# Performance work log

Hardware: AMD Instinct MI355X
Metric: run time of the kernel (lower is better)

## Reference

```python
import jax, jax.numpy as jnp
import numpy as np

LN_EPS = 1e-5


def setup_inputs() -> dict:
    key = jax.random.key(0)
    k1, k2, k3, k4, k5, k6 = jax.random.split(key, 6)
    B, S, P = 4, 4096, 16          # batch, seq_len, max_n_bytes
    LR, D = 256, 1024              # lowrank_dim, embedding_dim
    # byte ids in [-1, 255]; -1 marks missing bytes
    bytes_ids = jax.random.randint(k1, (B, S, P), -1, 256)
    byte_table = jax.random.normal(k2, (256, LR), dtype=jnp.float32) * 0.02
    pos_emb = jax.random.normal(k3, (P, LR, LR), dtype=jnp.float32)
    W_up = jax.random.normal(k4, (D, LR), dtype=jnp.float32) * 0.02
    b_up = jnp.zeros((D,), dtype=jnp.float32)
    ln_gamma = jnp.ones((D,), dtype=jnp.float32)
    ln_beta = jnp.zeros((D,), dtype=jnp.float32)
    return {
        "bytes_ids": bytes_ids,
        "byte_table": byte_table,
        "pos_emb": pos_emb,
        "W_up": W_up,
        "b_up": b_up,
        "ln_gamma": ln_gamma,
        "ln_beta": ln_beta,
    }


def reference(bytes_ids, byte_table, pos_emb, W_up, b_up, ln_gamma, ln_beta):
    # bytes_ids: [B, S, P] int, -1 => missing byte
    missing = bytes_ids == -1                             # [B,S,P]
    ids = jnp.where(missing, 0, bytes_ids)
    be = byte_table[ids]                                  # [B,S,P,LR] gather
    # per-position small matmul: pos_emb[p] applied to each byte embedding
    emb = jnp.einsum('pij,bspi->bspj', pos_emb, be)       # [B,S,P,LR]
    emb = jnp.where(missing[..., None], 0.0, emb)         # mask missing bytes
    emb = emb.sum(axis=-2)                                # [B,S,LR]
    x = emb @ W_up.T + b_up                               # [B,S,D]
    # layernorm
    mu = x.mean(axis=-1, keepdims=True)
    var = jnp.mean(jnp.square(x - mu), axis=-1, keepdims=True)
    return (x - mu) * jax.lax.rsqrt(var + LN_EPS) * ln_gamma + ln_beta
```

## Files before the change

kernel.cpp:

```cpp
#include <hip/hip_runtime.h>
#include <stdint.h>

#define PP     16
#define LRDIM  256
#define DDIM   1024
#define LN_EPS 1e-5f

typedef __attribute__((ext_vector_type(8))) short  short8;
typedef __attribute__((ext_vector_type(4))) float  f32x4;

__device__ __forceinline__ uint32_t bf16_rne(float f) {
    uint32_t u = __builtin_bit_cast(uint32_t, f);
    return (u + 0x7fffu + ((u >> 16) & 1u)) >> 16;
}
__device__ __forceinline__ float bf_lo(uint32_t u) {
    return __builtin_bit_cast(float, u << 16);
}
__device__ __forceinline__ float bf_hi(uint32_t u) {
    return __builtin_bit_cast(float, u & 0xffff0000u);
}

__global__ __launch_bounds__(256) void k_prep(const float* __restrict__ bt,
                                              const float* __restrict__ pe,
                                              const float* __restrict__ W,
                                              unsigned short* __restrict__ t2b,
                                              uint4* __restrict__ wb) {
    if (blockIdx.x < 512) {
        const int p  = blockIdx.x >> 5;
        const int c0 = (blockIdx.x & 31) << 3;
        const int j  = threadIdx.x;
        const float* pep = pe + (size_t)p * LRDIM * LRDIM;
        float a[8];
#pragma unroll
        for (int r = 0; r < 8; ++r) a[r] = 0.f;
#pragma unroll 4
        for (int i = 0; i < LRDIM; ++i) {
            const float v = pep[i * LRDIM + j];
#pragma unroll
            for (int r = 0; r < 8; ++r)
                a[r] = fmaf(v, bt[(c0 + r) * LRDIM + i], a[r]);
        }
#pragma unroll
        for (int r = 0; r < 8; ++r)
            t2b[(size_t)((p << 8) + c0 + r) * LRDIM + j] =
                (unsigned short)bf16_rne(a[r]);
    } else {
        const int gt  = (blockIdx.x - 512) * 256 + threadIdx.x;
        const int l   = gt & 63;
        const int ks  = (gt >> 6) & 7;
        const int nfg = gt >> 9;
        const int n   = nfg * 16 + (l & 15);
        const int k   = ks * 32 + (l >> 4) * 8;
        const float* src = W + (size_t)n * LRDIM + k;
        uint32_t r[4];
#pragma unroll
        for (int q = 0; q < 4; ++q) {
            const uint32_t lo = bf16_rne(src[2 * q + 0]);
            const uint32_t hi = bf16_rne(src[2 * q + 1]);
            r[q] = lo | (hi << 16);
        }
        wb[gt] = make_uint4(r[0], r[1], r[2], r[3]);
    }
}

__global__ __launch_bounds__(256) void k_gather(const int* __restrict__ ids,
                                                const unsigned short* __restrict__ t2b,
                                                uint2* __restrict__ Aq,
                                                int ntok) {
    const int wid = (blockIdx.x << 2) + (threadIdx.x >> 6);
    const int l   = threadIdx.x & 63;
    if (wid >= ntok) return;

    const int myid = (l < PP) ? ids[(size_t)wid * PP + l] : -1;

    float a0 = 0.f, a1 = 0.f, a2 = 0.f, a3 = 0.f;
#pragma unroll
    for (int p = 0; p < PP; ++p) {
        const int   id  = __shfl(myid, p);
        const float msk = (id >= 0) ? 1.f : 0.f;
        const uint2 v = *(const uint2*)(t2b +
                          ((size_t)((p << 8) + (id & 255)) << 8) + (l << 2));
        a0 = fmaf(msk, bf_lo(v.x), a0);
        a1 = fmaf(msk, bf_hi(v.x), a1);
        a2 = fmaf(msk, bf_lo(v.y), a2);
        a3 = fmaf(msk, bf_hi(v.y), a3);
    }
    uint2 pk;
    pk.x = bf16_rne(a0) | (bf16_rne(a1) << 16);
    pk.y = bf16_rne(a2) | (bf16_rne(a3) << 16);
    Aq[(size_t)wid * 64 + l] = pk;
}

__global__ __launch_bounds__(512, 4) void k_gemm(const unsigned short* __restrict__ A,
                                                 const uint4* __restrict__ wb,
                                                 const float* __restrict__ b_up,
                                                 const float* __restrict__ gamma,
                                                 const float* __restrict__ beta,
                                                 float* __restrict__ out,
                                                 int ntok) {
    __shared__ float ln_s[8][32];
    __shared__ float ln_ss[8][32];

    const int t    = threadIdx.x;
    const int w    = t >> 6;
    const int l    = t & 63;
    const int lo4  = l & 15;
    const int hi2  = l >> 4;
    const int tok0 = blockIdx.x << 5;

    f32x4 acc[2][8];
#pragma unroll
    for (int m2 = 0; m2 < 2; ++m2)
#pragma unroll
        for (int nf = 0; nf < 8; ++nf) {
            f32x4 z = {0.f, 0.f, 0.f, 0.f};
            acc[m2][nf] = z;
        }

    const unsigned short* Abase = A + ((size_t)tok0 << 8);

#pragma unroll
    for (int ks = 0; ks < 8; ++ks) {
        short8 af[2];
#pragma unroll
        for (int m2 = 0; m2 < 2; ++m2) {
            const int row = (m2 << 4) + lo4;
            af[m2] = *(const short8*)(Abase + ((size_t)row << 8) + (ks << 5) + (hi2 << 3));
        }
#pragma unroll
        for (int nf = 0; nf < 8; ++nf) {
            const int nfg = (w << 3) + nf;
            const uint4 bv = wb[(size_t)((nfg << 3) + ks) * 64 + l];
            const short8 bfr = __builtin_bit_cast(short8, bv);
            acc[0][nf] = __builtin_amdgcn_mfma_f32_16x16x32_bf16(af[0], bfr, acc[0][nf], 0, 0, 0);
            acc[1][nf] = __builtin_amdgcn_mfma_f32_16x16x32_bf16(af[1], bfr, acc[1][nf], 0, 0, 0);
        }
    }

    float s_[8], ss_[8];
#pragma unroll
    for (int q = 0; q < 8; ++q) { s_[q] = 0.f; ss_[q] = 0.f; }

#pragma unroll
    for (int nf = 0; nf < 8; ++nf) {
        const int col = (w << 7) + (nf << 4) + lo4;
        const float bu = b_up[col];
#pragma unroll
        for (int m2 = 0; m2 < 2; ++m2) {
            f32x4 v = acc[m2][nf];
            v.x += bu; v.y += bu; v.z += bu; v.w += bu;
            acc[m2][nf] = v;
            const int q0 = m2 * 4;
            s_[q0 + 0] += v.x; ss_[q0 + 0] += v.x * v.x;
            s_[q0 + 1] += v.y; ss_[q0 + 1] += v.y * v.y;
            s_[q0 + 2] += v.z; ss_[q0 + 2] += v.z * v.z;
            s_[q0 + 3] += v.w; ss_[q0 + 3] += v.w * v.w;
        }
    }
#pragma unroll
    for (int off = 1; off < 16; off <<= 1)
#pragma unroll
        for (int q = 0; q < 8; ++q) {
            s_[q]  += __shfl_xor(s_[q], off);
            ss_[q] += __shfl_xor(ss_[q], off);
        }
    if (lo4 == 0) {
#pragma unroll
        for (int q = 0; q < 8; ++q) {
            const int tl = (q >> 2) * 16 + hi2 * 4 + (q & 3);
            ln_s[w][tl]  = s_[q];
            ln_ss[w][tl] = ss_[q];
        }
    }
    __syncthreads();

    float mu_[8], inv_[8];
#pragma unroll
    for (int q = 0; q < 8; ++q) {
        const int tl = (q >> 2) * 16 + hi2 * 4 + (q & 3);
        float S = 0.f, SS = 0.f;
#pragma unroll
        for (int ww = 0; ww < 8; ++ww) { S += ln_s[ww][tl]; SS += ln_ss[ww][tl]; }
        const float mu  = S * (1.f / DDIM);
        const float var = SS * (1.f / DDIM) - mu * mu;
        mu_[q]  = mu;
        inv_[q] = rsqrtf(var + LN_EPS);
    }

#pragma unroll
    for (int nf = 0; nf < 8; ++nf) {
        const int col = (w << 7) + (nf << 4) + lo4;
        const float g  = gamma[col];
        const float bb = beta[col];
#pragma unroll
        for (int m2 = 0; m2 < 2; ++m2) {
            const f32x4 v = acc[m2][nf];
#pragma unroll
            for (int r = 0; r < 4; ++r) {
                const int q   = m2 * 4 + r;
                const int tl  = m2 * 16 + hi2 * 4 + r;
                const int tok = tok0 + tl;
                if (tok < ntok)
                    out[(size_t)tok * DDIM + col] = (v[r] - mu_[q]) * inv_[q] * g + bb;
            }
        }
    }
}

extern "C" void kernel_launch(void* const* d_in, const int* in_sizes, int n_in,
                              void* d_out, int out_size, void* d_ws, size_t ws_size,
                              hipStream_t stream) {
    const int*   ids   = (const int*)  d_in[0];
    const float* bt    = (const float*)d_in[1];
    const float* pe    = (const float*)d_in[2];
    const float* W     = (const float*)d_in[3];
    const float* b_up  = (const float*)d_in[4];
    const float* gamma = (const float*)d_in[5];
    const float* beta  = (const float*)d_in[6];
    float* out = (float*)d_out;

    const int ntok = in_sizes[0] / PP;

    char* ws = (char*)d_ws;
    unsigned short* t2b = (unsigned short*)(ws);
    uint4*          wbb = (uint4*)(ws + (2 << 20));
    unsigned short* Abf = (unsigned short*)(ws + (3 << 20));
    uint2*          Aq  = (uint2*)Abf;

    hipLaunchKernelGGL(k_prep, dim3(640), dim3(256), 0, stream, bt, pe, W, t2b, wbb);
    hipLaunchKernelGGL(k_gather, dim3((ntok + 3) / 4), dim3(256), 0, stream,
                       ids, t2b, Aq, ntok);
    hipLaunchKernelGGL(k_gemm, dim3((ntok + 31) / 32), dim3(512), 0, stream,
                       Abf, wbb, b_up, gamma, beta, out, ntok);
}
```

Measured before the change: 90.16 us.

## Split GEMM+LayerNorm into register-resident-W GEMM and separate LN kernel

The fused GEMM+LayerNorm kernel is split in two. The GEMM now covers half the output columns per block, preloads its B fragments into registers from a ks-major weight layout, and writes bf16 pre-norm activations to a workspace buffer. A separate row-wise LayerNorm kernel reads those activations and writes the fp32 output with vectorized stores. This aims to relieve register pressure and improve the GEMM's access pattern, but it adds a bf16 round trip through global memory, an extra launch, and an extra bf16 rounding before normalization.

```diff
diff --git a/kernel.cpp b/kernel.cpp
--- a/kernel.cpp
+++ b/kernel.cpp
@@ -59,7 +59,7 @@
             const uint32_t hi = bf16_rne(src[2 * q + 1]);
             r[q] = lo | (hi << 16);
         }
-        wb[gt] = make_uint4(r[0], r[1], r[2], r[3]);
+        wb[((ks << 6) + nfg) * 64 + l] = make_uint4(r[0], r[1], r[2], r[3]);
     }
 }
 
@@ -88,122 +88,115 @@
     uint2 pk;
     pk.x = bf16_rne(a0) | (bf16_rne(a1) << 16);
     pk.y = bf16_rne(a2) | (bf16_rne(a3) << 16);
-    Aq[(size_t)wid * 64 + l] = pk;
-}
-
-__global__ __launch_bounds__(512, 4) void k_gemm(const unsigned short* __restrict__ A,
-                                                 const uint4* __restrict__ wb,
-                                                 const float* __restrict__ b_up,
-                                                 const float* __restrict__ gamma,
-                                                 const float* __restrict__ beta,
-                                                 float* __restrict__ out,
-                                                 int ntok) {
-    __shared__ float ln_s[8][32];
-    __shared__ float ln_ss[8][32];
-
+    Aq[((size_t)wid << 6) + l] = pk;
+}
+
+__global__ __launch_bounds__(512, 2) void k_gemmB(const unsigned short* __restrict__ A,
+                                                  const uint4* __restrict__ wb,
+                                                  const float* __restrict__ b_up,
+                                                  unsigned short* __restrict__ x16,
+                                                  int ntok) {
     const int t    = threadIdx.x;
     const int w    = t >> 6;
     const int l    = t & 63;
     const int lo4  = l & 15;
     const int hi2  = l >> 4;
-    const int tok0 = blockIdx.x << 5;
-
-    f32x4 acc[2][8];
+    const int tile = blockIdx.x >> 1;
+    const int h    = blockIdx.x & 1;
+    const int tok0 = tile << 5;
+
+    uint4 breg[32];
+    const uint4* wp = wb + ((size_t)((h << 5) + (w << 2)) << 6) + l;
+#pragma unroll
+    for (int ks = 0; ks < 8; ++ks)
+#pragma unroll
+        for (int nf = 0; nf < 4; ++nf)
+            breg[ks * 4 + nf] = wp[(size_t)((ks << 6) + nf) << 6];
+
+    f32x4 acc[2][4];
 #pragma unroll
     for (int m2 = 0; m2 < 2; ++m2)
 #pragma unroll
-        for (int nf = 0; nf < 8; ++nf) {
+        for (int nf = 0; nf < 4; ++nf) {
             f32x4 z = {0.f, 0.f, 0.f, 0.f};
             acc[m2][nf] = z;
         }
 
     const unsigned short* Abase = A + ((size_t)tok0 << 8);
-
 #pragma unroll
     for (int ks = 0; ks < 8; ++ks) {
-        short8 af[2];
-#pragma unroll
-        for (int m2 = 0; m2 < 2; ++m2) {
-            const int row = (m2 << 4) + lo4;
-            af[m2] = *(const short8*)(Abase + ((size_t)row << 8) + (ks << 5) + (hi2 << 3));
-        }
-#pragma unroll
-        for (int nf = 0; nf < 8; ++nf) {
-            const int nfg = (w << 3) + nf;
-            const uint4 bv = wb[(size_t)((nfg << 3) + ks) * 64 + l];
-            const short8 bfr = __builtin_bit_cast(short8, bv);
-            acc[0][nf] = __builtin_amdgcn_mfma_f32_16x16x32_bf16(af[0], bfr, acc[0][nf], 0, 0, 0);
-            acc[1][nf] = __builtin_amdgcn_mfma_f32_16x16x32_bf16(af[1], bfr, acc[1][nf], 0, 0, 0);
-        }
-    }
-
-    float s_[8], ss_[8];
-#pragma unroll
-    for (int q = 0; q < 8; ++q) { s_[q] = 0.f; ss_[q] = 0.f; }
-
-#pragma unroll
-    for (int nf = 0; nf < 8; ++nf) {
-        const int col = (w << 7) + (nf << 4) + lo4;
+        const short8 af0 = *(const short8*)(Abase + ((size_t)lo4 << 8) +
+                                            (ks << 5) + (hi2 << 3));
+        const short8 af1 = *(const short8*)(Abase + ((size_t)(16 + lo4) << 8) +
+                                            (ks << 5) + (hi2 << 3));
+#pragma unroll
+        for (int nf = 0; nf < 4; ++nf) {
+            const short8 bfr = __builtin_bit_cast(short8, breg[ks * 4 + nf]);
+            acc[0][nf] = __builtin_amdgcn_mfma_f32_16x16x32_bf16(af0, bfr, acc[0][nf], 0, 0, 0);
+            acc[1][nf] = __builtin_amdgcn_mfma_f32_16x16x32_bf16(af1, bfr, acc[1][nf], 0, 0, 0);
+        }
+    }
+
+#pragma unroll
+    for (int nf = 0; nf < 4; ++nf) {
+        const int col = (h << 9) + (w << 6) + (nf << 4) + lo4;
         const float bu = b_up[col];
-#pragma unroll
-        for (int m2 = 0; m2 < 2; ++m2) {
-            f32x4 v = acc[m2][nf];
-            v.x += bu; v.y += bu; v.z += bu; v.w += bu;
-            acc[m2][nf] = v;
-            const int q0 = m2 * 4;
-            s_[q0 + 0] += v.x; ss_[q0 + 0] += v.x * v.x;
-            s_[q0 + 1] += v.y; ss_[q0 + 1] += v.y * v.y;
-            s_[q0 + 2] += v.z; ss_[q0 + 2] += v.z * v.z;
-            s_[q0 + 3] += v.w; ss_[q0 + 3] += v.w * v.w;
-        }
-    }
-#pragma unroll
-    for (int off = 1; off < 16; off <<= 1)
-#pragma unroll
-        for (int q = 0; q < 8; ++q) {
-            s_[q]  += __shfl_xor(s_[q], off);
-            ss_[q] += __shfl_xor(ss_[q], off);
-        }
-    if (lo4 == 0) {
-#pragma unroll
-        for (int q = 0; q < 8; ++q) {
-            const int tl = (q >> 2) * 16 + hi2 * 4 + (q & 3);
-            ln_s[w][tl]  = s_[q];
-            ln_ss[w][tl] = ss_[q];
-        }
-    }
-    __syncthreads();
-
-    float mu_[8], inv_[8];
-#pragma unroll
-    for (int q = 0; q < 8; ++q) {
-        const int tl = (q >> 2) * 16 + hi2 * 4 + (q & 3);
-        float S = 0.f, SS = 0.f;
-#pragma unroll
-        for (int ww = 0; ww < 8; ++ww) { S += ln_s[ww][tl]; SS += ln_ss[ww][tl]; }
-        const float mu  = S * (1.f / DDIM);
-        const float var = SS * (1.f / DDIM) - mu * mu;
-        mu_[q]  = mu;
-        inv_[q] = rsqrtf(var + LN_EPS);
-    }
-
-#pragma unroll
-    for (int nf = 0; nf < 8; ++nf) {
-        const int col = (w << 7) + (nf << 4) + lo4;
-        const float g  = gamma[col];
-        const float bb = beta[col];
 #pragma unroll
         for (int m2 = 0; m2 < 2; ++m2) {
             const f32x4 v = acc[m2][nf];
 #pragma unroll
             for (int r = 0; r < 4; ++r) {
-                const int q   = m2 * 4 + r;
-                const int tl  = m2 * 16 + hi2 * 4 + r;
-                const int tok = tok0 + tl;
+                const int tok = tok0 + (m2 << 4) + (hi2 << 2) + r;
                 if (tok < ntok)
-                    out[(size_t)tok * DDIM + col] = (v[r] - mu_[q]) * inv_[q] * g + bb;
+                    x16[((size_t)tok << 10) + col] =
+                        (unsigned short)bf16_rne(v[r] + bu);
             }
         }
+    }
+}
+
+__global__ __launch_bounds__(256) void k_ln(const unsigned short* __restrict__ x16,
+                                            const float* __restrict__ gamma,
+                                            const float* __restrict__ beta,
+                                            float* __restrict__ out,
+                                            int ntok) {
+    const int row = (blockIdx.x << 2) + (threadIdx.x >> 6);
+    const int l   = threadIdx.x & 63;
+    if (row >= ntok) return;
+
+    const unsigned short* xr = x16 + ((size_t)row << 10);
+    float v[16];
+#pragma unroll
+    for (int q = 0; q < 4; ++q) {
+        const uint2 u = *(const uint2*)(xr + (q << 8) + (l << 2));
+        v[q * 4 + 0] = bf_lo(u.x);
+        v[q * 4 + 1] = bf_hi(u.x);
+        v[q * 4 + 2] = bf_lo(u.y);
+        v[q * 4 + 3] = bf_hi(u.y);
+    }
+    float s = 0.f, ss = 0.f;
+#pragma unroll
+    for (int k = 0; k < 16; ++k) { s += v[k]; ss += v[k] * v[k]; }
+#pragma unroll
+    for (int off = 1; off < 64; off <<= 1) {
+        s  += __shfl_xor(s, off);
+        ss += __shfl_xor(ss, off);
+    }
+    const float mu  = s * (1.f / DDIM);
+    const float var = ss * (1.f / DDIM) - mu * mu;
+    const float inv = rsqrtf(var + LN_EPS);
+
+    float* orow = out + ((size_t)row << 10);
+#pragma unroll
+    for (int q = 0; q < 4; ++q) {
+        const float4 g  = ((const float4*)gamma)[(q << 6) + l];
+        const float4 be = ((const float4*)beta)[(q << 6) + l];
+        float4 o;
+        o.x = (v[q * 4 + 0] - mu) * inv * g.x + be.x;
+        o.y = (v[q * 4 + 1] - mu) * inv * g.y + be.y;
+        o.z = (v[q * 4 + 2] - mu) * inv * g.z + be.z;
+        o.w = (v[q * 4 + 3] - mu) * inv * g.w + be.w;
+        ((float4*)orow)[(q << 6) + l] = o;
     }
 }
 
@@ -223,13 +216,16 @@
 
     char* ws = (char*)d_ws;
     unsigned short* t2b = (unsigned short*)(ws);
-    uint4*          wbb = (uint4*)(ws + (2 << 20));
-    unsigned short* Abf = (unsigned short*)(ws + (3 << 20));
+    uint4*          wbb = (uint4*)(ws + (2  << 20));
+    unsigned short* Abf = (unsigned short*)(ws + (3  << 20));
     uint2*          Aq  = (uint2*)Abf;
+    unsigned short* x16 = (unsigned short*)(ws + (11 << 20));
 
     hipLaunchKernelGGL(k_prep, dim3(640), dim3(256), 0, stream, bt, pe, W, t2b, wbb);
     hipLaunchKernelGGL(k_gather, dim3((ntok + 3) / 4), dim3(256), 0, stream,
                        ids, t2b, Aq, ntok);
-    hipLaunchKernelGGL(k_gemm, dim3((ntok + 31) / 32), dim3(512), 0, stream,
-                       Abf, wbb, b_up, gamma, beta, out, ntok);
-}
+    hipLaunchKernelGGL(k_gemmB, dim3((ntok + 31) / 32 * 2), dim3(512), 0, stream,
+                       Abf, wbb, b_up, x16, ntok);
+    hipLaunchKernelGGL(k_ln, dim3((ntok + 3) / 4), dim3(256), 0, stream,
+                       x16, gamma, beta, out, ntok);
+}
```

Result: slower. 92.61 us (+2.7%).
